# Kernel tuning notes

Measured on AMD Instinct MI355X. Metric: run time of the kernel, lower is better.

Reference implementation:

```python
import jax, jax.numpy as jnp
import numpy as np

N_NODES = 100000
N_EDGES = 1600000
DIM_IN, DIM_H, DIM_OUT = 64, 64, 16


def setup_inputs() -> dict:
    key = jax.random.key(0)
    ks = jax.random.split(key, 7)
    s = lambda d: 1.0 / np.sqrt(d)
    return {
        "x": jax.random.normal(ks[0], (N_NODES, DIM_IN), dtype=jnp.float32),
        "edge_index": jax.random.randint(ks[1], (2, N_EDGES), 0, N_NODES, dtype=jnp.int32),
        "W1l": jax.random.normal(ks[2], (DIM_IN, DIM_H), dtype=jnp.float32) * s(DIM_IN),
        "W1r": jax.random.normal(ks[3], (DIM_IN, DIM_H), dtype=jnp.float32) * s(DIM_IN),
        "b1": jnp.zeros((DIM_H,), dtype=jnp.float32),
        "W2l": jax.random.normal(ks[4], (DIM_H, DIM_OUT), dtype=jnp.float32) * s(DIM_H),
        "W2r": jax.random.normal(ks[5], (DIM_H, DIM_OUT), dtype=jnp.float32) * s(DIM_H),
        "b2": jnp.zeros((DIM_OUT,), dtype=jnp.float32),
    }


def _sage_conv(h, edge_index, Wl, Wr, b):
    # PyG SAGEConv (mean aggr): out = mean_{j in N(i)} h_j @ Wl + h_i @ Wr + b
    src, dst = edge_index[0], edge_index[1]
    n = h.shape[0]
    agg = jax.ops.segment_sum(h[src], dst, num_segments=n)          # [N, d]
    deg = jax.ops.segment_sum(jnp.ones_like(dst, dtype=h.dtype), dst, num_segments=n)
    mean = agg / jnp.maximum(deg, 1.0)[:, None]
    return mean @ Wl + h @ Wr + b


def reference(x, edge_index, W1l, W1r, b1, W2l, W2r, b2):
    h = jax.nn.relu(_sage_conv(x, edge_index, W1l, W1r, b1))
    # dropout(p=0.5) is identity in eval mode (training=False)
    h = _sage_conv(h, edge_index, W2l, W2r, b2)
    return jax.nn.log_softmax(h, axis=1)
```

## Files before the change

### kernel.cpp

```cpp
#include <hip/hip_runtime.h>
#include <cstdint>
#include <cstddef>


typedef float f32x4 __attribute__((ext_vector_type(4)));
typedef float f32x2 __attribute__((ext_vector_type(2)));
typedef short short8 __attribute__((ext_vector_type(8)));
typedef __bf16 bf16x8 __attribute__((ext_vector_type(8)));

#define BK 256
#define NBMAX 512
#define CAP 5120
#define TILE 8192

__device__ __forceinline__ unsigned f2bf(float f) {
    unsigned u = __float_as_uint(f);
    u += 0x7FFFu + ((u >> 16) & 1u);
    return u >> 16;
}

__device__ __forceinline__ f32x4 mfma16(short8 a, short8 b, f32x4 c) {
    return __builtin_amdgcn_mfma_f32_16x16x32_bf16(
        __builtin_bit_cast(bf16x8, a), __builtin_bit_cast(bf16x8, b), c, 0, 0, 0);
}

#define ACC2(r, alo, ahi)                     \
    alo += __uint_as_float((r) << 16);        \
    ahi += __uint_as_float(r);

#define ACCF8(w, i)                                                   \
    {                                                                 \
        f32x2 f0 = __builtin_amdgcn_cvt_pk_f32_fp8((w), false);       \
        f32x2 f1 = __builtin_amdgcn_cvt_pk_f32_fp8((w), true);        \
        acc[(i)] += f0.x; acc[(i) + 1] += f0.y;                       \
        acc[(i) + 2] += f1.x; acc[(i) + 3] += f1.y;                   \
    }

__global__ __launch_bounds__(512) void partprep_k(
    const int* __restrict__ ei, int* __restrict__ bcnt,
    unsigned* __restrict__ part, int E, int pblocks,
    const float* __restrict__ x, unsigned short* __restrict__ xb,
    unsigned char* __restrict__ xq, int n,
    const float* __restrict__ W1l, const float* __restrict__ W1r,
    const float* __restrict__ W2l, const float* __restrict__ W2r,
    unsigned short* __restrict__ bimg, int xblocks) {
    __shared__ int scn[NBMAX], sbase[NBMAX], lofs[NBMAX], cur[NBMAX];
    __shared__ unsigned stageW[TILE];
    __shared__ unsigned short stageB[TILE];
    int t = threadIdx.x;
    int bid = blockIdx.x;

    if (bid >= pblocks) {
        int cb = bid - pblocks;
        if (cb < xblocks) {
            int i = (cb * 512 + t) * 8;
            if (i >= n) return;
            const float4* xp = (const float4*)(x + i);
            float4 a = xp[0], b = xp[1];
            uint4 o;
            o.x = f2bf(a.x) | (f2bf(a.y) << 16);
            o.y = f2bf(a.z) | (f2bf(a.w) << 16);
            o.z = f2bf(b.x) | (f2bf(b.y) << 16);
            o.w = f2bf(b.z) | (f2bf(b.w) << 16);
            *(uint4*)(xb + i) = o;
            int w0 = __builtin_amdgcn_cvt_pk_fp8_f32(a.x, a.y, 0, false);
            w0 = __builtin_amdgcn_cvt_pk_fp8_f32(a.z, a.w, w0, true);
            int w1 = __builtin_amdgcn_cvt_pk_fp8_f32(b.x, b.y, 0, false);
            w1 = __builtin_amdgcn_cvt_pk_fp8_f32(b.z, b.w, w1, true);
            *(uint2*)(xq + i) = make_uint2((unsigned)w0, (unsigned)w1);
            return;
        }
        int e = (cb - xblocks) * 512 + t;
        if (e >= 20 * 64) return;
        int f = e >> 6, L = e & 63;
        int qd = L >> 4, m = L & 15;
        unsigned o[8];
        if (f < 16) {
            int kb = f >> 2, nb = f & 3;
            int n2 = nb * 16 + m;
#pragma unroll
            for (int j = 0; j < 8; ++j) {
                int k = kb * 32 + qd * 8 + j;
                float v = (k < 64) ? W1l[k * 64 + n2] : W1r[(k - 64) * 64 + n2];
                o[j] = f2bf(v);
            }
        } else {
            int g = f - 16;
            int kb = g >> 1, nb = g & 1;
#pragma unroll
            for (int j = 0; j < 8; ++j) {
                int k = kb * 32 + qd * 8 + j;
                float v = nb ? W2r[k * 16 + m] : W2l[k * 16 + m];
                o[j] = f2bf(v);
            }
        }
        uint4 pk;
        pk.x = o[0] | (o[1] << 16);
        pk.y = o[2] | (o[3] << 16);
        pk.z = o[4] | (o[5] << 16);
        pk.w = o[6] | (o[7] << 16);
        ((uint4*)bimg)[e] = pk;
        return;
    }

    int base = bid * TILE;
    cur[t] = 0;
    __syncthreads();
    int4 s4[4], d4[4];
#pragma unroll
    for (int i = 0; i < 4; ++i) {
        int e0 = base + (t + i * 512) * 4;
        if (e0 < E) {
            s4[i] = ((const int4*)ei)[e0 >> 2];
            d4[i] = ((const int4*)(ei + E))[e0 >> 2];
        } else {
            d4[i] = make_int4(-1, -1, -1, -1);
            s4[i] = make_int4(0, 0, 0, 0);
        }
    }
    int rk[16];
#pragma unroll
    for (int i = 0; i < 4; ++i) {
        int d[4] = {d4[i].x, d4[i].y, d4[i].z, d4[i].w};
#pragma unroll
        for (int u = 0; u < 4; ++u)
            rk[i * 4 + u] = (d[u] >= 0) ? atomicAdd(&cur[d[u] >> 8], 1) : 0;
    }
    __syncthreads();
    int own = cur[t];
    scn[t] = own;
    __syncthreads();
    for (int off = 1; off < NBMAX; off <<= 1) {
        int v = (t >= off) ? scn[t - off] : 0;
        __syncthreads();
        scn[t] += v;
        __syncthreads();
    }
    lofs[t] = scn[t] - own;
    if (own > 0) sbase[t] = atomicAdd(&bcnt[t], own);
    __syncthreads();
#pragma unroll
    for (int i = 0; i < 4; ++i) {
        int s[4] = {s4[i].x, s4[i].y, s4[i].z, s4[i].w};
        int d[4] = {d4[i].x, d4[i].y, d4[i].z, d4[i].w};
#pragma unroll
        for (int u = 0; u < 4; ++u) {
            if (d[u] < 0) continue;
            int b = d[u] >> 8;
            int pos = lofs[b] + rk[i * 4 + u];
            stageW[pos] = ((unsigned)(d[u] & (BK - 1)) << 17) | (unsigned)s[u];
            stageB[pos] = (unsigned short)b;
        }
    }
    __syncthreads();
    int tot = scn[NBMAX - 1];
    for (int q = t; q < tot; q += 512) {
        int b = stageB[q];
        part[b * CAP + sbase[b] + (q - lofs[b])] = stageW[q];
    }
}

__global__ __launch_bounds__(256) void csr_k(const unsigned* __restrict__ part,
                                             const int* __restrict__ bcnt,
                                             int* __restrict__ csr,
                                             int2* __restrict__ rowse, int N) {
    __shared__ int h[BK];
    __shared__ int s[BK];
    int b = blockIdx.x, t = threadIdx.x;
    int cnt = bcnt[b];
    int base = b * CAP;
    h[t] = 0;
    __syncthreads();
    for (int q = t; q < cnt; q += 256)
        atomicAdd(&h[(part[base + q] >> 17) & (BK - 1)], 1);
    __syncthreads();
    int own = h[t];
    s[t] = own;
    __syncthreads();
    for (int off = 1; off < BK; off <<= 1) {
        int v = (t >= off) ? s[t - off] : 0;
        __syncthreads();
        s[t] += v;
        __syncthreads();
    }
    int excl = s[t] - own;
    int node = b * BK + t;
    if (node < N) rowse[node] = make_int2(base + excl, base + excl + own);
    __syncthreads();
    h[t] = excl;
    __syncthreads();
    for (int q = t; q < cnt; q += 256) {
        unsigned w = part[base + q];
        int pos = atomicAdd(&h[(w >> 17) & (BK - 1)], 1);
        csr[base + pos] = (int)(w & 0x1FFFFu);
    }
}

__global__ __launch_bounds__(256, 6) void l1x(
    const unsigned short* __restrict__ xb, const unsigned char* __restrict__ xq,
    const int2* __restrict__ rowse, const int* __restrict__ csr,
    const unsigned short* __restrict__ bimg,
    const float* __restrict__ b1, const float* __restrict__ b2,
    unsigned short* __restrict__ p, float* __restrict__ q, int N) {
    __shared__ unsigned short mh[4][16][72];
    int t = threadIdx.x;
    int wave = t >> 6, lane = t & 63;
    int nodebase = blockIdx.x * 64 + wave * 16;
    int grp = lane >> 2, sub = lane & 3;
    int node = nodebase + grp;
    int2 be = (node < N) ? rowse[node] : make_int2(0, 0);

    float acc[16];
#pragma unroll
    for (int i = 0; i < 16; ++i) acc[i] = 0.f;
    int k = be.x, kend = be.y;
    for (; k + 1 < kend; k += 2) {
        int src0 = csr[k], src1 = csr[k + 1];
        uint4 a = ((const uint4*)(xq + ((size_t)src0 << 6)))[sub];
        uint4 b = ((const uint4*)(xq + ((size_t)src1 << 6)))[sub];
        ACCF8(a.x, 0); ACCF8(a.y, 4); ACCF8(a.z, 8); ACCF8(a.w, 12);
        ACCF8(b.x, 0); ACCF8(b.y, 4); ACCF8(b.z, 8); ACCF8(b.w, 12);
    }
    if (k < kend) {
        int src0 = csr[k];
        uint4 a = ((const uint4*)(xq + ((size_t)src0 << 6)))[sub];
        ACCF8(a.x, 0); ACCF8(a.y, 4); ACCF8(a.z, 8); ACCF8(a.w, 12);
    }
    {
        float rd = 1.0f / fmaxf((float)(be.y - be.x), 1.0f);
        uint4 o0, o1;
        o0.x = f2bf(acc[0] * rd) | (f2bf(acc[1] * rd) << 16);
        o0.y = f2bf(acc[2] * rd) | (f2bf(acc[3] * rd) << 16);
        o0.z = f2bf(acc[4] * rd) | (f2bf(acc[5] * rd) << 16);
        o0.w = f2bf(acc[6] * rd) | (f2bf(acc[7] * rd) << 16);
        o1.x = f2bf(acc[8] * rd) | (f2bf(acc[9] * rd) << 16);
        o1.y = f2bf(acc[10] * rd) | (f2bf(acc[11] * rd) << 16);
        o1.z = f2bf(acc[12] * rd) | (f2bf(acc[13] * rd) << 16);
        o1.w = f2bf(acc[14] * rd) | (f2bf(acc[15] * rd) << 16);
        *(uint4*)&mh[wave][grp][sub * 16] = o0;
        *(uint4*)&mh[wave][grp][sub * 16 + 8] = o1;
    }

    int qd = lane >> 4, m = lane & 15;
    int mynode = nodebase + m;
    const short8* bfr = (const short8*)bimg;
    short8 afr0 = *(const short8*)&mh[wave][m][qd * 8];
    short8 afr1 = *(const short8*)&mh[wave][m][32 + qd * 8];
    short8 afr2 = {0, 0, 0, 0, 0, 0, 0, 0};
    short8 afr3 = {0, 0, 0, 0, 0, 0, 0, 0};
    if (mynode < N) {
        afr2 = *(const short8*)(xb + ((size_t)mynode << 6) + qd * 8);
        afr3 = *(const short8*)(xb + ((size_t)mynode << 6) + 32 + qd * 8);
    }

#pragma unroll
    for (int nb = 0; nb < 4; ++nb) {
        f32x4 c = {0.f, 0.f, 0.f, 0.f};
        c = mfma16(afr0, bfr[nb * 64 + lane], c);
        c = mfma16(afr1, bfr[(4 + nb) * 64 + lane], c);
        c = mfma16(afr2, bfr[(8 + nb) * 64 + lane], c);
        c = mfma16(afr3, bfr[(12 + nb) * 64 + lane], c);
        int col = nb * 16 + m;
        float bb = b1[col];
#pragma unroll
        for (int r = 0; r < 4; ++r) {
            float hv = fmaxf(c[r] + bb, 0.0f);
            mh[wave][qd * 4 + r][col] = (unsigned short)f2bf(hv);
        }
    }

    short8 ha0 = *(const short8*)&mh[wave][m][qd * 8];
    short8 ha1 = *(const short8*)&mh[wave][m][32 + qd * 8];
    f32x4 pc = {0.f, 0.f, 0.f, 0.f}, qc = {0.f, 0.f, 0.f, 0.f};
    pc = mfma16(ha0, bfr[16 * 64 + lane], pc);
    pc = mfma16(ha1, bfr[18 * 64 + lane], pc);
    qc = mfma16(ha0, bfr[17 * 64 + lane], qc);
    qc = mfma16(ha1, bfr[19 * 64 + lane], qc);
    float b2v = b2[m];
#pragma unroll
    for (int r = 0; r < 4; ++r) {
        int nd = nodebase + qd * 4 + r;
        if (nd < N) {
            p[(size_t)nd * 16 + m] = (unsigned short)f2bf(pc[r]);
            q[(size_t)nd * 16 + m] = qc[r] + b2v;
        }
    }
}

__global__ __launch_bounds__(256) void finalk(const unsigned short* __restrict__ p,
                                              const int2* __restrict__ rowse,
                                              const int* __restrict__ csr,
                                              float* q, int N) {
    int t = threadIdx.x;
    int wave = t >> 6, lane = t & 63;
    int grp = lane >> 2, sub = lane & 3;
    int node = blockIdx.x * 64 + wave * 16 + grp;
    if (node >= N) return;
    int2 be = rowse[node];
    float a0 = 0.f, a1 = 0.f, a2 = 0.f, a3 = 0.f;
    int k = be.x, kend = be.y;
    for (; k + 1 < kend; k += 2) {
        int src0 = csr[k], src1 = csr[k + 1];
        uint2 rA = *(const uint2*)(p + ((size_t)src0 << 4) + (sub << 2));
        uint2 rB = *(const uint2*)(p + ((size_t)src1 << 4) + (sub << 2));
        ACC2(rA.x, a0, a1);  ACC2(rA.y, a2, a3);
        ACC2(rB.x, a0, a1);  ACC2(rB.y, a2, a3);
    }
    if (k < kend) {
        int src0 = csr[k];
        uint2 rA = *(const uint2*)(p + ((size_t)src0 << 4) + (sub << 2));
        ACC2(rA.x, a0, a1);  ACC2(rA.y, a2, a3);
    }
    float rd = 1.0f / fmaxf((float)(be.y - be.x), 1.0f);
    float4 qv = ((const float4*)(q + ((size_t)node << 4)))[sub];
    float4 v = {a0 * rd + qv.x, a1 * rd + qv.y, a2 * rd + qv.z, a3 * rd + qv.w};
    float mm = fmaxf(fmaxf(v.x, v.y), fmaxf(v.z, v.w));
    mm = fmaxf(mm, __shfl_xor(mm, 1));
    mm = fmaxf(mm, __shfl_xor(mm, 2));
    float s = __expf(v.x - mm) + __expf(v.y - mm) + __expf(v.z - mm) + __expf(v.w - mm);
    s += __shfl_xor(s, 1);
    s += __shfl_xor(s, 2);
    float ls = __logf(s);
    float4 o = {v.x - mm - ls, v.y - mm - ls, v.z - mm - ls, v.w - mm - ls};
    ((float4*)(q + ((size_t)node << 4)))[sub] = o;
}

extern "C" void kernel_launch(void* const* d_in, const int* in_sizes, int n_in,
                              void* d_out, int out_size, void* d_ws, size_t ws_size,
                              hipStream_t stream) {
    const float* x   = (const float*)d_in[0];
    const int* ei    = (const int*)d_in[1];
    const float* W1l = (const float*)d_in[2];
    const float* W1r = (const float*)d_in[3];
    const float* b1  = (const float*)d_in[4];
    const float* W2l = (const float*)d_in[5];
    const float* W2r = (const float*)d_in[6];
    const float* b2  = (const float*)d_in[7];
    const int N = in_sizes[0] / 64;
    const int E = in_sizes[1] / 2;
    const int nbk = (N + BK - 1) / BK;

    int*  bcnt  = (int*)d_ws;
    int2* rowse = (int2*)(bcnt + NBMAX);
    int*  csr   = (int*)(rowse + N);
    unsigned short* bimg = (unsigned short*)(csr + (size_t)nbk * CAP);
    unsigned short* p    = bimg + 20 * 64 * 8;
    unsigned* part = (unsigned*)(p + (size_t)N * 16);
    unsigned short* xb = (unsigned short*)(part + (size_t)nbk * CAP);
    unsigned char* xq = (unsigned char*)(xb + (size_t)N * 64);
    float* q = (float*)d_out;

    hipMemsetAsync(bcnt, 0, NBMAX * sizeof(int), stream);

    const int pblocks = (E + TILE - 1) / TILE;
    const int xblocks = (N * 64 + 4095) / 4096;
    partprep_k<<<pblocks + xblocks + 3, 512, 0, stream>>>(
        ei, bcnt, part, E, pblocks, x, xb, xq, N * 64, W1l, W1r, W2l, W2r,
        bimg, xblocks);
    csr_k<<<nbk, 256, 0, stream>>>(part, bcnt, csr, rowse, N);
    l1x<<<(N + 63) / 64, 256, 0, stream>>>(xb, xq, rowse, csr, bimg, b1, b2,
                                           p, q, N);
    finalk<<<(N + 63) / 64, 256, 0, stream>>>(p, rowse, csr, q, N);
}
```

Baseline: 160.1 us.

## Degree-sort nodes within each bucket to balance gather loops across lanes

csr_k now builds a per-bucket counting sort of nodes by in-degree (clamped at 63) and writes a byte permutation. l1x and finalk use it to map each lane group to a node, so the 16 nodes handled by one wave have similar degrees and the divergent gather loops waste fewer idle lanes. Grids are resized to cover whole buckets, which adds a few padding blocks. finalk's neighbour loop is also unrolled by four to keep more loads in flight. The cost is an extra shared-memory histogram and scan in csr_k and scattered output writes.

```diff
diff --git a/kernel.cpp b/kernel.cpp
--- a/kernel.cpp
+++ b/kernel.cpp
@@ -163,19 +163,25 @@
 __global__ __launch_bounds__(256) void csr_k(const unsigned* __restrict__ part,
                                              const int* __restrict__ bcnt,
                                              int* __restrict__ csr,
-                                             int2* __restrict__ rowse, int N) {
+                                             int2* __restrict__ rowse,
+                                             unsigned char* __restrict__ ord,
+                                             int N) {
     __shared__ int h[BK];
     __shared__ int s[BK];
+    __shared__ int dh[64], dcur[64];
     int b = blockIdx.x, t = threadIdx.x;
     int cnt = bcnt[b];
     int base = b * CAP;
     h[t] = 0;
+    if (t < 64) dh[t] = 0;
     __syncthreads();
     for (int q = t; q < cnt; q += 256)
         atomicAdd(&h[(part[base + q] >> 17) & (BK - 1)], 1);
     __syncthreads();
     int own = h[t];
     s[t] = own;
+    int dcl = own < 63 ? own : 63;
+    atomicAdd(&dh[dcl], 1);
     __syncthreads();
     for (int off = 1; off < BK; off <<= 1) {
         int v = (t >= off) ? s[t - off] : 0;
@@ -183,22 +189,35 @@
         s[t] += v;
         __syncthreads();
     }
+    if (t < 64) {
+        int v = dh[t];
+        int sc = v;
+#pragma unroll
+        for (int off = 1; off < 64; off <<= 1) {
+            int u = __shfl_up(sc, off);
+            if (t >= off) sc += u;
+        }
+        dcur[t] = sc - v;
+    }
     int excl = s[t] - own;
     int node = b * BK + t;
     if (node < N) rowse[node] = make_int2(base + excl, base + excl + own);
     __syncthreads();
+    int pos = atomicAdd(&dcur[dcl], 1);
+    ord[b * BK + pos] = (unsigned char)t;
     h[t] = excl;
     __syncthreads();
     for (int q = t; q < cnt; q += 256) {
         unsigned w = part[base + q];
-        int pos = atomicAdd(&h[(w >> 17) & (BK - 1)], 1);
-        csr[base + pos] = (int)(w & 0x1FFFFu);
+        int ps = atomicAdd(&h[(w >> 17) & (BK - 1)], 1);
+        csr[base + ps] = (int)(w & 0x1FFFFu);
     }
 }
 
 __global__ __launch_bounds__(256, 6) void l1x(
     const unsigned short* __restrict__ xb, const unsigned char* __restrict__ xq,
     const int2* __restrict__ rowse, const int* __restrict__ csr,
+    const unsigned char* __restrict__ ord,
     const unsigned short* __restrict__ bimg,
     const float* __restrict__ b1, const float* __restrict__ b2,
     unsigned short* __restrict__ p, float* __restrict__ q, int N) {
@@ -206,8 +225,11 @@
     int t = threadIdx.x;
     int wave = t >> 6, lane = t & 63;
     int nodebase = blockIdx.x * 64 + wave * 16;
+    int bb = nodebase & ~(BK - 1);
     int grp = lane >> 2, sub = lane & 3;
-    int node = nodebase + grp;
+    int qd = lane >> 4, m = lane & 15;
+    int ordm = ord[nodebase + m];
+    int node = bb | __shfl(ordm, grp);
     int2 be = (node < N) ? rowse[node] : make_int2(0, 0);
 
     float acc[16];
@@ -241,8 +263,7 @@
         *(uint4*)&mh[wave][grp][sub * 16 + 8] = o1;
     }
 
-    int qd = lane >> 4, m = lane & 15;
-    int mynode = nodebase + m;
+    int mynode = bb | ordm;
     const short8* bfr = (const short8*)bimg;
     short8 afr0 = *(const short8*)&mh[wave][m][qd * 8];
     short8 afr1 = *(const short8*)&mh[wave][m][32 + qd * 8];
@@ -261,10 +282,10 @@
         c = mfma16(afr2, bfr[(8 + nb) * 64 + lane], c);
         c = mfma16(afr3, bfr[(12 + nb) * 64 + lane], c);
         int col = nb * 16 + m;
-        float bb = b1[col];
+        float bb1 = b1[col];
 #pragma unroll
         for (int r = 0; r < 4; ++r) {
-            float hv = fmaxf(c[r] + bb, 0.0f);
+            float hv = fmaxf(c[r] + bb1, 0.0f);
             mh[wave][qd * 4 + r][col] = (unsigned short)f2bf(hv);
         }
     }
@@ -279,7 +300,7 @@
     float b2v = b2[m];
 #pragma unroll
     for (int r = 0; r < 4; ++r) {
-        int nd = nodebase + qd * 4 + r;
+        int nd = bb | __shfl(ordm, qd * 4 + r);
         if (nd < N) {
             p[(size_t)nd * 16 + m] = (unsigned short)f2bf(pc[r]);
             q[(size_t)nd * 16 + m] = qc[r] + b2v;
@@ -290,25 +311,31 @@
 __global__ __launch_bounds__(256) void finalk(const unsigned short* __restrict__ p,
                                               const int2* __restrict__ rowse,
                                               const int* __restrict__ csr,
+                                              const unsigned char* __restrict__ ord,
                                               float* q, int N) {
     int t = threadIdx.x;
     int wave = t >> 6, lane = t & 63;
     int grp = lane >> 2, sub = lane & 3;
-    int node = blockIdx.x * 64 + wave * 16 + grp;
+    int posi = blockIdx.x * 64 + wave * 16 + grp;
+    int node = (posi & ~(BK - 1)) | ord[posi];
     if (node >= N) return;
     int2 be = rowse[node];
     float a0 = 0.f, a1 = 0.f, a2 = 0.f, a3 = 0.f;
     int k = be.x, kend = be.y;
-    for (; k + 1 < kend; k += 2) {
-        int src0 = csr[k], src1 = csr[k + 1];
-        uint2 rA = *(const uint2*)(p + ((size_t)src0 << 4) + (sub << 2));
-        uint2 rB = *(const uint2*)(p + ((size_t)src1 << 4) + (sub << 2));
+    for (; k + 3 < kend; k += 4) {
+        int s0 = csr[k], s1 = csr[k + 1], s2 = csr[k + 2], s3 = csr[k + 3];
+        uint2 rA = *(const uint2*)(p + ((size_t)s0 << 4) + (sub << 2));
+        uint2 rB = *(const uint2*)(p + ((size_t)s1 << 4) + (sub << 2));
+        uint2 rC = *(const uint2*)(p + ((size_t)s2 << 4) + (sub << 2));
+        uint2 rD = *(const uint2*)(p + ((size_t)s3 << 4) + (sub << 2));
         ACC2(rA.x, a0, a1);  ACC2(rA.y, a2, a3);
         ACC2(rB.x, a0, a1);  ACC2(rB.y, a2, a3);
-    }
-    if (k < kend) {
-        int src0 = csr[k];
-        uint2 rA = *(const uint2*)(p + ((size_t)src0 << 4) + (sub << 2));
+        ACC2(rC.x, a0, a1);  ACC2(rC.y, a2, a3);
+        ACC2(rD.x, a0, a1);  ACC2(rD.y, a2, a3);
+    }
+    for (; k < kend; ++k) {
+        int s0 = csr[k];
+        uint2 rA = *(const uint2*)(p + ((size_t)s0 << 4) + (sub << 2));
         ACC2(rA.x, a0, a1);  ACC2(rA.y, a2, a3);
     }
     float rd = 1.0f / fmaxf((float)(be.y - be.x), 1.0f);
@@ -348,6 +375,7 @@
     unsigned* part = (unsigned*)(p + (size_t)N * 16);
     unsigned short* xb = (unsigned short*)(part + (size_t)nbk * CAP);
     unsigned char* xq = (unsigned char*)(xb + (size_t)N * 64);
+    unsigned char* ordb = xq + (size_t)N * 64;
     float* q = (float*)d_out;
 
     hipMemsetAsync(bcnt, 0, NBMAX * sizeof(int), stream);
@@ -357,8 +385,8 @@
     partprep_k<<<pblocks + xblocks + 3, 512, 0, stream>>>(
         ei, bcnt, part, E, pblocks, x, xb, xq, N * 64, W1l, W1r, W2l, W2r,
         bimg, xblocks);
-    csr_k<<<nbk, 256, 0, stream>>>(part, bcnt, csr, rowse, N);
-    l1x<<<(N + 63) / 64, 256, 0, stream>>>(xb, xq, rowse, csr, bimg, b1, b2,
-                                           p, q, N);
-    finalk<<<(N + 63) / 64, 256, 0, stream>>>(p, rowse, csr, q, N);
-}
+    csr_k<<<nbk, 256, 0, stream>>>(part, bcnt, csr, rowse, ordb, N);
+    l1x<<<nbk * 4, 256, 0, stream>>>(xb, xq, rowse, csr, ordb, bimg, b1, b2,
+                                     p, q, N);
+    finalk<<<nbk * 4, 256, 0, stream>>>(p, rowse, csr, ordb, q, N);
+}
```

Result: slower. 177.8 us (+11.1%).
